# Performance work log

Measured on AMD Instinct MI355X. Metric: run time of the kernel, lower is better.

## Reference

```python
import jax, jax.numpy as jnp
import numpy as np

N = 100000
E = 3200000
D_IN = 128
D_OUT = 128
ALPHA = 0.2  # LeakyReLU negative slope
LN_EPS = 1e-5


def setup_inputs() -> dict:
    key = jax.random.key(0)
    k1, k2, k3, k4, k5 = jax.random.split(key, 5)
    x = jax.random.normal(k1, (N, D_IN), dtype=jnp.float32)
    edge = jax.random.randint(k2, (2, E), 0, N, dtype=jnp.int64)
    # Linear params (kaiming-normal-ish init)
    W = jax.random.normal(k3, (D_OUT, D_IN), dtype=jnp.float32) * np.sqrt(2.0 / D_IN)
    b = jnp.zeros((D_OUT,), dtype=jnp.float32)
    # attention vector a: (2*out,)
    a = jax.random.normal(k4, (2 * D_OUT,), dtype=jnp.float32) * np.sqrt(2.0 / (2 * D_OUT))
    ln_w = jnp.ones((D_OUT,), dtype=jnp.float32)
    ln_b = jnp.zeros((D_OUT,), dtype=jnp.float32)
    return {"x": x, "W": W, "b": b, "a": a, "ln_w": ln_w, "ln_b": ln_b, "edge": edge}


def reference(x, W, b, a, ln_w, ln_b, edge):
    n = x.shape[0]
    d_out = W.shape[0]
    h = x @ W.T + b  # [N, D_OUT]
    src, dst = edge[0], edge[1]
    # a.mm(cat(h[src], h[dst]).T) == h[src] @ a1 + h[dst] @ a2
    a1, a2 = a[:d_out], a[d_out:]
    node_s1 = h @ a1  # [N]
    node_s2 = h @ a2  # [N]
    z = node_s1[src] + node_s2[dst]  # [E]
    edge_e = jnp.exp(-jax.nn.leaky_relu(z, ALPHA))  # [E]
    # sparse spmm: h_prime[i] = sum_{e: src=i} edge_e[e] * h[dst[e]]
    msgs = edge_e[:, None] * h[dst]  # [E, D_OUT]
    h_prime = jax.ops.segment_sum(msgs, src, num_segments=n)  # [N, D_OUT]
    # LayerNorm over last dim
    mu = jnp.mean(h_prime, axis=-1, keepdims=True)
    var = jnp.mean(jnp.square(h_prime - mu), axis=-1, keepdims=True)
    h_norm = (h_prime - mu) * jax.lax.rsqrt(var + LN_EPS) * ln_w + ln_b
    return jax.nn.elu(h_norm)
```

## Files before the change

### kernel.cpp

```cpp
#include <hip/hip_runtime.h>
#include <math.h>

#define D 128
#define GAT_ALPHA 0.2f
#define LN_EPS 1e-5f
#define NBMAX 400
#define CAP 9216
#define ECHUNK 16384
#define XPITCH 136

typedef __attribute__((ext_vector_type(8))) short short8;
typedef __attribute__((ext_vector_type(4))) float floatx4;

__device__ __forceinline__ unsigned short f2bf(float f) {
    unsigned u = __float_as_uint(f);
    unsigned r = (u + 0x7fffu + ((u >> 16) & 1u)) >> 16;
    return (unsigned short)r;
}
__device__ __forceinline__ float bfl(unsigned u) { return __uint_as_float(u << 16); }
__device__ __forceinline__ float bfh(unsigned u) { return __uint_as_float(u & 0xffff0000u); }

__global__ __launch_bounds__(256) void prep_bfrag(const float* __restrict__ W,
                                                  unsigned short* __restrict__ Bfrag)
{
    for (int idx = threadIdx.x; idx < 2048; idx += 256) {
        int lane = idx & 63, ntkt = idx >> 6;
        int nt = ntkt >> 2, kt = ntkt & 3;
        int l16 = lane & 15, quad = lane >> 4;
        const float* wp = W + (size_t)(nt * 16 + l16) * D + kt * 32 + quad * 8;
        unsigned short* op = Bfrag + (size_t)idx * 8;
#pragma unroll
        for (int j = 0; j < 8; ++j) op[j] = f2bf(wp[j]);
    }
}

__global__ __launch_bounds__(256) void gemm_mfma(const float* __restrict__ x,
                                                 const unsigned short* __restrict__ Bfrag_g,
                                                 const float* __restrict__ b,
                                                 const float* __restrict__ a,
                                                 unsigned short* __restrict__ h16,
                                                 float* __restrict__ s1,
                                                 float* __restrict__ s2, int n)
{
    __shared__ unsigned short Bf[16384];
    __shared__ unsigned short xs[64 * XPITCH];
    const int tid = threadIdx.x;
    {
        const uint2* sp = (const uint2*)Bfrag_g;
        uint2* dp = (uint2*)Bf;
        for (int i = tid; i < 4096; i += 256) dp[i] = sp[i];
    }
    const int row0 = blockIdx.x * 64;

    for (int i = tid; i < 2048; i += 256) {
        int row = i >> 5, c4 = i & 31;
        float4 v = make_float4(0.f, 0.f, 0.f, 0.f);
        if (row0 + row < n) v = *(const float4*)(x + (size_t)(row0 + row) * D + c4 * 4);
        ushort4 o;
        o.x = f2bf(v.x); o.y = f2bf(v.y); o.z = f2bf(v.z); o.w = f2bf(v.w);
        *(ushort4*)&xs[row * XPITCH + c4 * 4] = o;
    }
    __syncthreads();

    const int lane = tid & 63, wave = tid >> 6;
    const int l16 = lane & 15, quad = lane >> 4;

    floatx4 acc[8];
#pragma unroll
    for (int nt = 0; nt < 8; ++nt) acc[nt] = (floatx4){0.f, 0.f, 0.f, 0.f};

#pragma unroll
    for (int kt = 0; kt < 4; ++kt) {
        short8 af = *(const short8*)&xs[(wave * 16 + l16) * XPITCH + kt * 32 + quad * 8];
#pragma unroll
        for (int nt = 0; nt < 8; ++nt) {
            short8 bf = *(const short8*)&Bf[(size_t)((nt * 4 + kt) * 64 + lane) * 8];
            acc[nt] = __builtin_amdgcn_mfma_f32_16x16x32_bf16(af, bf, acc[nt], 0, 0, 0);
        }
    }

    float bcol[8], a1c[8], a2c[8];
#pragma unroll
    for (int nt = 0; nt < 8; ++nt) {
        int c = nt * 16 + l16;
        bcol[nt] = b[c]; a1c[nt] = a[c]; a2c[nt] = a[D + c];
    }
    float hv[4][8];
#pragma unroll
    for (int r = 0; r < 4; ++r) {
        float p1 = 0.f, p2 = 0.f;
#pragma unroll
        for (int nt = 0; nt < 8; ++nt) {
            float v = acc[nt][r] + bcol[nt];
            hv[r][nt] = v;
            p1 = fmaf(v, a1c[nt], p1);
            p2 = fmaf(v, a2c[nt], p2);
        }
#pragma unroll
        for (int off = 8; off > 0; off >>= 1) {
            p1 += __shfl_xor(p1, off);
            p2 += __shfl_xor(p2, off);
        }
        int crow = row0 + wave * 16 + quad * 4 + r;
        if (crow < n && l16 == 0) { s1[crow] = p1; s2[crow] = p2; }
    }

    __syncthreads();
#pragma unroll
    for (int r = 0; r < 4; ++r)
#pragma unroll
        for (int nt = 0; nt < 8; ++nt)
            xs[(wave * 16 + quad * 4 + r) * XPITCH + nt * 16 + l16] = f2bf(hv[r][nt]);
    __syncthreads();

    for (int i = tid; i < 1024; i += 256) {
        int row = i >> 4, c = i & 15;
        if (row0 + row < n)
            *(uint4*)(h16 + (size_t)(row0 + row) * D + c * 8) =
                *(const uint4*)&xs[row * XPITCH + c * 8];
    }
}

__global__ __launch_bounds__(512) void partition_kernel(const int* __restrict__ src,
                                                        const int* __restrict__ dst,
                                                        int* __restrict__ gcnt,
                                                        int* __restrict__ pairs,
                                                        int nE, int nb)
{
    __shared__ int cnt[NBMAX], basex[NBMAX], cnt2[NBMAX];
    int tid = threadIdx.x;
    for (int i = tid; i < nb; i += 512) { cnt[i] = 0; cnt2[i] = 0; }
    __syncthreads();
    int e0 = blockIdx.x * ECHUNK;
    int e1 = e0 + ECHUNK; if (e1 > nE) e1 = nE;
    for (int e = e0 + tid; e < e1; e += 512)
        atomicAdd(&cnt[src[e] >> 8], 1);
    __syncthreads();
    for (int i = tid; i < nb; i += 512)
        basex[i] = cnt[i] ? atomicAdd(&gcnt[i], cnt[i]) : 0;
    __syncthreads();
    for (int e = e0 + tid; e < e1; e += 512) {
        int s = src[e];
        int bb = s >> 8;
        int l = basex[bb] + atomicAdd(&cnt2[bb], 1);
        if (l < CAP) pairs[(size_t)bb * CAP + l] = ((s & 255) << 24) | dst[e];
    }
}

__global__ __launch_bounds__(256) void bucket_sort(const int* __restrict__ pairs,
                                                   const int* __restrict__ gcnt,
                                                   const float* __restrict__ s1,
                                                   const float* __restrict__ s2,
                                                   int* __restrict__ beg,
                                                   int* __restrict__ end_,
                                                   int2* __restrict__ csr, int n)
{
    __shared__ int cnt[256], excl[256], cnt2[256], wsum[4];
    int bkt = blockIdx.x, tid = threadIdx.x;
    int base = bkt * CAP;
    int m = gcnt[bkt]; if (m > CAP) m = CAP;
    cnt[tid] = 0; cnt2[tid] = 0;
    __syncthreads();
    for (int e = tid; e < m; e += 256)
        atomicAdd(&cnt[((unsigned)pairs[base + e]) >> 24], 1);
    __syncthreads();

    int lane = tid & 63, wid = tid >> 6;
    int v = cnt[tid], incl = v;
#pragma unroll
    for (int off = 1; off < 64; off <<= 1) {
        int t = __shfl_up(incl, off);
        if (lane >= off) incl += t;
    }
    if (lane == 63) wsum[wid] = incl;
    __syncthreads();
    int woff = 0;
#pragma unroll
    for (int w = 0; w < 4; ++w)
        if (w < wid) woff += wsum[w];
    int ex = woff + incl - v;
    excl[tid] = ex;
    int node = bkt * 256 + tid;
    if (node < n) { beg[node] = base + ex; end_[node] = base + ex + v; }
    __syncthreads();

    for (int e = tid; e < m; e += 256) {
        int w = pairs[base + e];
        int sl = ((unsigned)w) >> 24;
        int d = w & 0xFFFFFF;
        int s = (bkt << 8) | sl;
        float z = s1[s] + s2[d];
        float lz = z > 0.f ? z : GAT_ALPHA * z;
        float ee = __expf(-lz);
        int pos = excl[sl] + atomicAdd(&cnt2[sl], 1);
        csr[base + pos] = make_int2(d, __float_as_int(ee));
    }
}

__global__ __launch_bounds__(256) void aggregate_kernel(const unsigned short* __restrict__ h16,
                                                        const int* __restrict__ beg,
                                                        const int* __restrict__ end_,
                                                        const int2* __restrict__ csr,
                                                        const float* __restrict__ ln_w,
                                                        const float* __restrict__ ln_b,
                                                        float* __restrict__ out, int n)
{
    int node = blockIdx.x * 4 + (threadIdx.x >> 6);
    if (node >= n) return;
    int lane = threadIdx.x & 63;
    int q    = lane >> 4;
    int l16  = lane & 15;

    int e0 = beg[node], e1 = end_[node];

    float acc[8];
#pragma unroll
    for (int j = 0; j < 8; ++j) acc[j] = 0.f;

    int e = e0 + q;
    for (; e + 4 < e1; e += 8) {
        int2 pa = csr[e];
        int2 pb = csr[e + 4];
        const uint4* gpa = (const uint4*)(h16 + (size_t)pa.x * D + l16 * 8);
        const uint4* gpb = (const uint4*)(h16 + (size_t)pb.x * D + l16 * 8);
        uint4 ua = *gpa;
        uint4 ub = *gpb;
        float ea = __int_as_float(pa.y);
        float eb = __int_as_float(pb.y);
        acc[0] = fmaf(ea, bfl(ua.x), acc[0]);
        acc[1] = fmaf(ea, bfh(ua.x), acc[1]);
        acc[2] = fmaf(ea, bfl(ua.y), acc[2]);
        acc[3] = fmaf(ea, bfh(ua.y), acc[3]);
        acc[4] = fmaf(ea, bfl(ua.z), acc[4]);
        acc[5] = fmaf(ea, bfh(ua.z), acc[5]);
        acc[6] = fmaf(ea, bfl(ua.w), acc[6]);
        acc[7] = fmaf(ea, bfh(ua.w), acc[7]);
        acc[0] = fmaf(eb, bfl(ub.x), acc[0]);
        acc[1] = fmaf(eb, bfh(ub.x), acc[1]);
        acc[2] = fmaf(eb, bfl(ub.y), acc[2]);
        acc[3] = fmaf(eb, bfh(ub.y), acc[3]);
        acc[4] = fmaf(eb, bfl(ub.z), acc[4]);
        acc[5] = fmaf(eb, bfh(ub.z), acc[5]);
        acc[6] = fmaf(eb, bfl(ub.w), acc[6]);
        acc[7] = fmaf(eb, bfh(ub.w), acc[7]);
    }
    for (; e < e1; e += 4) {
        int2 p = csr[e];
        float ee = __int_as_float(p.y);
        uint4 u = *(const uint4*)(h16 + (size_t)p.x * D + l16 * 8);
        acc[0] = fmaf(ee, bfl(u.x), acc[0]);
        acc[1] = fmaf(ee, bfh(u.x), acc[1]);
        acc[2] = fmaf(ee, bfl(u.y), acc[2]);
        acc[3] = fmaf(ee, bfh(u.y), acc[3]);
        acc[4] = fmaf(ee, bfl(u.z), acc[4]);
        acc[5] = fmaf(ee, bfh(u.z), acc[5]);
        acc[6] = fmaf(ee, bfl(u.w), acc[6]);
        acc[7] = fmaf(ee, bfh(u.w), acc[7]);
    }
#pragma unroll
    for (int j = 0; j < 8; ++j) acc[j] += __shfl_down(acc[j], 32);
#pragma unroll
    for (int j = 0; j < 8; ++j) acc[j] += __shfl_down(acc[j], 16);

    float sum = 0.f, sq = 0.f;
#pragma unroll
    for (int j = 0; j < 8; ++j) { sum += acc[j]; sq += acc[j] * acc[j]; }
#pragma unroll
    for (int off = 8; off > 0; off >>= 1) {
        sum += __shfl_xor(sum, off);
        sq  += __shfl_xor(sq, off);
    }

    if (q == 0) {
        float mu   = sum * (1.0f / 128.0f);
        float var  = sq * (1.0f / 128.0f) - mu * mu;
        float rstd = rsqrtf(var + LN_EPS);

        float4 w0 = *(const float4*)(ln_w + l16 * 8);
        float4 w1 = *(const float4*)(ln_w + l16 * 8 + 4);
        float4 b0 = *(const float4*)(ln_b + l16 * 8);
        float4 b1 = *(const float4*)(ln_b + l16 * 8 + 4);
        float y[8];
        y[0] = (acc[0] - mu) * rstd * w0.x + b0.x;
        y[1] = (acc[1] - mu) * rstd * w0.y + b0.y;
        y[2] = (acc[2] - mu) * rstd * w0.z + b0.z;
        y[3] = (acc[3] - mu) * rstd * w0.w + b0.w;
        y[4] = (acc[4] - mu) * rstd * w1.x + b1.x;
        y[5] = (acc[5] - mu) * rstd * w1.y + b1.y;
        y[6] = (acc[6] - mu) * rstd * w1.z + b1.z;
        y[7] = (acc[7] - mu) * rstd * w1.w + b1.w;
#pragma unroll
        for (int j = 0; j < 8; ++j) y[j] = y[j] > 0.f ? y[j] : expm1f(y[j]);
        float* op = out + (size_t)node * D + l16 * 8;
        *(float4*)op       = make_float4(y[0], y[1], y[2], y[3]);
        *(float4*)(op + 4) = make_float4(y[4], y[5], y[6], y[7]);
    }
}

extern "C" void kernel_launch(void* const* d_in, const int* in_sizes, int n_in,
                              void* d_out, int out_size, void* d_ws, size_t ws_size,
                              hipStream_t stream)
{
    const float* x    = (const float*)d_in[0];
    const float* W    = (const float*)d_in[1];
    const float* b    = (const float*)d_in[2];
    const float* a    = (const float*)d_in[3];
    const float* ln_w = (const float*)d_in[4];
    const float* ln_b = (const float*)d_in[5];
    const int*   edge = (const int*)d_in[6];

    const int n  = in_sizes[0] / D;
    const int nE = in_sizes[6] / 2;
    const int* src = edge;
    const int* dst = edge + nE;
    const int nb = (n + 255) >> 8;

    float* out = (float*)d_out;

    unsigned short* h16 = (unsigned short*)d_ws;
    float* s1   = (float*)(h16 + (size_t)n * D);
    float* s2   = s1 + n;
    unsigned short* Bfrag = (unsigned short*)(s2 + n);
    int* pairs  = (int*)(Bfrag + 16384);
    int2* csr   = (int2*)(pairs + (size_t)nb * CAP);
    int* beg    = (int*)(csr + (size_t)nb * CAP);
    int* end_   = beg + n;
    int* gcnt   = end_ + n;

    hipMemsetAsync(gcnt, 0, (size_t)nb * sizeof(int), stream);

    prep_bfrag      <<<1, 256, 0, stream>>>(W, Bfrag);
    gemm_mfma       <<<(n + 63) / 64, 256, 0, stream>>>(x, Bfrag, b, a, h16, s1, s2, n);
    partition_kernel<<<(nE + ECHUNK - 1) / ECHUNK, 512, 0, stream>>>(src, dst, gcnt, pairs, nE, nb);
    bucket_sort     <<<nb, 256, 0, stream>>>(pairs, gcnt, s1, s2, beg, end_, csr, n);
    aggregate_kernel<<<(n + 3) / 4, 256, 0, stream>>>(h16, beg, end_, csr, ln_w, ln_b, out, n);
}
```

Before: 362.7 us.

## Fuse bucket sort with aggregation using LDS-resident CSR and 128-node buckets

Merges the bucket_sort and aggregate kernels into a single kernel per 128-node bucket. Each block builds the sorted edge list in shared memory and then aggregates, normalises and writes the output for its nodes. This drops the global CSR write and read, the beg/end arrays and one launch, and caches s1 for the bucket in shared memory. The GEMM also now processes two 64-row tiles per block so each block loads the B fragments once for both. The costs are a large LDS footprint per block (about 38KB), fewer resident blocks (782 buckets), and a per-bucket capacity of 4736 edges that overflows if a bucket receives more edges than that.

```diff
diff --git a/kernel.cpp b/kernel.cpp
--- a/kernel.cpp
+++ b/kernel.cpp
@@ -4,8 +4,8 @@
 #define D 128
 #define GAT_ALPHA 0.2f
 #define LN_EPS 1e-5f
-#define NBMAX 400
-#define CAP 9216
+#define NB2MAX 800
+#define CAP2 4736
 #define ECHUNK 16384
 #define XPITCH 136
 
@@ -50,34 +50,8 @@
         uint2* dp = (uint2*)Bf;
         for (int i = tid; i < 4096; i += 256) dp[i] = sp[i];
     }
-    const int row0 = blockIdx.x * 64;
-
-    for (int i = tid; i < 2048; i += 256) {
-        int row = i >> 5, c4 = i & 31;
-        float4 v = make_float4(0.f, 0.f, 0.f, 0.f);
-        if (row0 + row < n) v = *(const float4*)(x + (size_t)(row0 + row) * D + c4 * 4);
-        ushort4 o;
-        o.x = f2bf(v.x); o.y = f2bf(v.y); o.z = f2bf(v.z); o.w = f2bf(v.w);
-        *(ushort4*)&xs[row * XPITCH + c4 * 4] = o;
-    }
-    __syncthreads();
-
     const int lane = tid & 63, wave = tid >> 6;
     const int l16 = lane & 15, quad = lane >> 4;
-
-    floatx4 acc[8];
-#pragma unroll
-    for (int nt = 0; nt < 8; ++nt) acc[nt] = (floatx4){0.f, 0.f, 0.f, 0.f};
-
-#pragma unroll
-    for (int kt = 0; kt < 4; ++kt) {
-        short8 af = *(const short8*)&xs[(wave * 16 + l16) * XPITCH + kt * 32 + quad * 8];
-#pragma unroll
-        for (int nt = 0; nt < 8; ++nt) {
-            short8 bf = *(const short8*)&Bf[(size_t)((nt * 4 + kt) * 64 + lane) * 8];
-            acc[nt] = __builtin_amdgcn_mfma_f32_16x16x32_bf16(af, bf, acc[nt], 0, 0, 0);
-        }
-    }
 
     float bcol[8], a1c[8], a2c[8];
 #pragma unroll
@@ -85,39 +59,69 @@
         int c = nt * 16 + l16;
         bcol[nt] = b[c]; a1c[nt] = a[c]; a2c[nt] = a[D + c];
     }
-    float hv[4][8];
-#pragma unroll
-    for (int r = 0; r < 4; ++r) {
-        float p1 = 0.f, p2 = 0.f;
-#pragma unroll
-        for (int nt = 0; nt < 8; ++nt) {
-            float v = acc[nt][r] + bcol[nt];
-            hv[r][nt] = v;
-            p1 = fmaf(v, a1c[nt], p1);
-            p2 = fmaf(v, a2c[nt], p2);
-        }
-#pragma unroll
-        for (int off = 8; off > 0; off >>= 1) {
-            p1 += __shfl_xor(p1, off);
-            p2 += __shfl_xor(p2, off);
-        }
-        int crow = row0 + wave * 16 + quad * 4 + r;
-        if (crow < n && l16 == 0) { s1[crow] = p1; s2[crow] = p2; }
-    }
-
-    __syncthreads();
-#pragma unroll
-    for (int r = 0; r < 4; ++r)
-#pragma unroll
-        for (int nt = 0; nt < 8; ++nt)
-            xs[(wave * 16 + quad * 4 + r) * XPITCH + nt * 16 + l16] = f2bf(hv[r][nt]);
-    __syncthreads();
-
-    for (int i = tid; i < 1024; i += 256) {
-        int row = i >> 4, c = i & 15;
-        if (row0 + row < n)
-            *(uint4*)(h16 + (size_t)(row0 + row) * D + c * 8) =
-                *(const uint4*)&xs[row * XPITCH + c * 8];
+
+    for (int t = 0; t < 2; ++t) {
+        const int row0 = blockIdx.x * 128 + t * 64;
+        __syncthreads();
+
+        for (int i = tid; i < 2048; i += 256) {
+            int row = i >> 5, c4 = i & 31;
+            float4 v = make_float4(0.f, 0.f, 0.f, 0.f);
+            if (row0 + row < n) v = *(const float4*)(x + (size_t)(row0 + row) * D + c4 * 4);
+            ushort4 o;
+            o.x = f2bf(v.x); o.y = f2bf(v.y); o.z = f2bf(v.z); o.w = f2bf(v.w);
+            *(ushort4*)&xs[row * XPITCH + c4 * 4] = o;
+        }
+        __syncthreads();
+
+        floatx4 acc[8];
+#pragma unroll
+        for (int nt = 0; nt < 8; ++nt) acc[nt] = (floatx4){0.f, 0.f, 0.f, 0.f};
+
+#pragma unroll
+        for (int kt = 0; kt < 4; ++kt) {
+            short8 af = *(const short8*)&xs[(wave * 16 + l16) * XPITCH + kt * 32 + quad * 8];
+#pragma unroll
+            for (int nt = 0; nt < 8; ++nt) {
+                short8 bf = *(const short8*)&Bf[(size_t)((nt * 4 + kt) * 64 + lane) * 8];
+                acc[nt] = __builtin_amdgcn_mfma_f32_16x16x32_bf16(af, bf, acc[nt], 0, 0, 0);
+            }
+        }
+
+        float hv[4][8];
+#pragma unroll
+        for (int r = 0; r < 4; ++r) {
+            float p1 = 0.f, p2 = 0.f;
+#pragma unroll
+            for (int nt = 0; nt < 8; ++nt) {
+                float v = acc[nt][r] + bcol[nt];
+                hv[r][nt] = v;
+                p1 = fmaf(v, a1c[nt], p1);
+                p2 = fmaf(v, a2c[nt], p2);
+            }
+#pragma unroll
+            for (int off = 8; off > 0; off >>= 1) {
+                p1 += __shfl_xor(p1, off);
+                p2 += __shfl_xor(p2, off);
+            }
+            int crow = row0 + wave * 16 + quad * 4 + r;
+            if (crow < n && l16 == 0) { s1[crow] = p1; s2[crow] = p2; }
+        }
+
+        __syncthreads();
+#pragma unroll
+        for (int r = 0; r < 4; ++r)
+#pragma unroll
+            for (int nt = 0; nt < 8; ++nt)
+                xs[(wave * 16 + quad * 4 + r) * XPITCH + nt * 16 + l16] = f2bf(hv[r][nt]);
+        __syncthreads();
+
+        for (int i = tid; i < 1024; i += 256) {
+            int row = i >> 4, c = i & 15;
+            if (row0 + row < n)
+                *(uint4*)(h16 + (size_t)(row0 + row) * D + c * 8) =
+                    *(const uint4*)&xs[row * XPITCH + c * 8];
+        }
     }
 }
 
@@ -127,173 +131,174 @@
                                                         int* __restrict__ pairs,
                                                         int nE, int nb)
 {
-    __shared__ int cnt[NBMAX], basex[NBMAX], cnt2[NBMAX];
+    __shared__ int cnt[NB2MAX], basex[NB2MAX], cnt2x[NB2MAX];
     int tid = threadIdx.x;
-    for (int i = tid; i < nb; i += 512) { cnt[i] = 0; cnt2[i] = 0; }
+    for (int i = tid; i < nb; i += 512) { cnt[i] = 0; cnt2x[i] = 0; }
     __syncthreads();
     int e0 = blockIdx.x * ECHUNK;
     int e1 = e0 + ECHUNK; if (e1 > nE) e1 = nE;
     for (int e = e0 + tid; e < e1; e += 512)
-        atomicAdd(&cnt[src[e] >> 8], 1);
+        atomicAdd(&cnt[src[e] >> 7], 1);
     __syncthreads();
     for (int i = tid; i < nb; i += 512)
         basex[i] = cnt[i] ? atomicAdd(&gcnt[i], cnt[i]) : 0;
     __syncthreads();
     for (int e = e0 + tid; e < e1; e += 512) {
         int s = src[e];
-        int bb = s >> 8;
-        int l = basex[bb] + atomicAdd(&cnt2[bb], 1);
-        if (l < CAP) pairs[(size_t)bb * CAP + l] = ((s & 255) << 24) | dst[e];
-    }
-}
-
-__global__ __launch_bounds__(256) void bucket_sort(const int* __restrict__ pairs,
-                                                   const int* __restrict__ gcnt,
-                                                   const float* __restrict__ s1,
-                                                   const float* __restrict__ s2,
-                                                   int* __restrict__ beg,
-                                                   int* __restrict__ end_,
-                                                   int2* __restrict__ csr, int n)
-{
-    __shared__ int cnt[256], excl[256], cnt2[256], wsum[4];
-    int bkt = blockIdx.x, tid = threadIdx.x;
-    int base = bkt * CAP;
-    int m = gcnt[bkt]; if (m > CAP) m = CAP;
-    cnt[tid] = 0; cnt2[tid] = 0;
-    __syncthreads();
-    for (int e = tid; e < m; e += 256)
+        int bb = s >> 7;
+        int l = basex[bb] + atomicAdd(&cnt2x[bb], 1);
+        if (l < CAP2) pairs[(size_t)bb * CAP2 + l] = ((s & 127) << 24) | dst[e];
+    }
+}
+
+__global__ __launch_bounds__(512, 8) void sort_aggregate(const int* __restrict__ pairs,
+                                                         const int* __restrict__ gcnt,
+                                                         const float* __restrict__ s1,
+                                                         const float* __restrict__ s2,
+                                                         const unsigned short* __restrict__ h16,
+                                                         const float* __restrict__ ln_w,
+                                                         const float* __restrict__ ln_b,
+                                                         float* __restrict__ out, int n)
+{
+    __shared__ int2 csr2[CAP2];
+    __shared__ int cnt[128], cnt2[128], excl[129];
+    __shared__ float sA[128];
+    __shared__ int wsum[2];
+
+    const int bkt = blockIdx.x, tid = threadIdx.x;
+    const int base = bkt * CAP2;
+    int m = gcnt[bkt]; if (m > CAP2) m = CAP2;
+
+    if (tid < 128) {
+        cnt[tid] = 0; cnt2[tid] = 0;
+        int node = bkt * 128 + tid;
+        sA[tid] = (node < n) ? s1[node] : 0.f;
+    }
+    __syncthreads();
+
+    for (int e = tid; e < m; e += 512)
         atomicAdd(&cnt[((unsigned)pairs[base + e]) >> 24], 1);
     __syncthreads();
 
-    int lane = tid & 63, wid = tid >> 6;
-    int v = cnt[tid], incl = v;
-#pragma unroll
-    for (int off = 1; off < 64; off <<= 1) {
-        int t = __shfl_up(incl, off);
-        if (lane >= off) incl += t;
-    }
-    if (lane == 63) wsum[wid] = incl;
-    __syncthreads();
-    int woff = 0;
-#pragma unroll
-    for (int w = 0; w < 4; ++w)
-        if (w < wid) woff += wsum[w];
-    int ex = woff + incl - v;
-    excl[tid] = ex;
-    int node = bkt * 256 + tid;
-    if (node < n) { beg[node] = base + ex; end_[node] = base + ex + v; }
-    __syncthreads();
-
-    for (int e = tid; e < m; e += 256) {
+    {
+        int lane = tid & 63, wid = tid >> 6;
+        int v = 0, incl = 0;
+        if (tid < 128) {
+            v = cnt[tid]; incl = v;
+#pragma unroll
+            for (int off = 1; off < 64; off <<= 1) {
+                int t = __shfl_up(incl, off);
+                if (lane >= off) incl += t;
+            }
+            if (lane == 63) wsum[wid] = incl;
+        }
+        __syncthreads();
+        if (tid < 128) excl[tid] = ((wid == 1) ? wsum[0] : 0) + incl - v;
+        if (tid == 0) excl[128] = wsum[0] + wsum[1];
+        __syncthreads();
+    }
+
+    for (int e = tid; e < m; e += 512) {
         int w = pairs[base + e];
         int sl = ((unsigned)w) >> 24;
         int d = w & 0xFFFFFF;
-        int s = (bkt << 8) | sl;
-        float z = s1[s] + s2[d];
+        float z = sA[sl] + s2[d];
         float lz = z > 0.f ? z : GAT_ALPHA * z;
         float ee = __expf(-lz);
         int pos = excl[sl] + atomicAdd(&cnt2[sl], 1);
-        csr[base + pos] = make_int2(d, __float_as_int(ee));
-    }
-}
-
-__global__ __launch_bounds__(256) void aggregate_kernel(const unsigned short* __restrict__ h16,
-                                                        const int* __restrict__ beg,
-                                                        const int* __restrict__ end_,
-                                                        const int2* __restrict__ csr,
-                                                        const float* __restrict__ ln_w,
-                                                        const float* __restrict__ ln_b,
-                                                        float* __restrict__ out, int n)
-{
-    int node = blockIdx.x * 4 + (threadIdx.x >> 6);
-    if (node >= n) return;
-    int lane = threadIdx.x & 63;
-    int q    = lane >> 4;
-    int l16  = lane & 15;
-
-    int e0 = beg[node], e1 = end_[node];
-
-    float acc[8];
-#pragma unroll
-    for (int j = 0; j < 8; ++j) acc[j] = 0.f;
-
-    int e = e0 + q;
-    for (; e + 4 < e1; e += 8) {
-        int2 pa = csr[e];
-        int2 pb = csr[e + 4];
-        const uint4* gpa = (const uint4*)(h16 + (size_t)pa.x * D + l16 * 8);
-        const uint4* gpb = (const uint4*)(h16 + (size_t)pb.x * D + l16 * 8);
-        uint4 ua = *gpa;
-        uint4 ub = *gpb;
-        float ea = __int_as_float(pa.y);
-        float eb = __int_as_float(pb.y);
-        acc[0] = fmaf(ea, bfl(ua.x), acc[0]);
-        acc[1] = fmaf(ea, bfh(ua.x), acc[1]);
-        acc[2] = fmaf(ea, bfl(ua.y), acc[2]);
-        acc[3] = fmaf(ea, bfh(ua.y), acc[3]);
-        acc[4] = fmaf(ea, bfl(ua.z), acc[4]);
-        acc[5] = fmaf(ea, bfh(ua.z), acc[5]);
-        acc[6] = fmaf(ea, bfl(ua.w), acc[6]);
-        acc[7] = fmaf(ea, bfh(ua.w), acc[7]);
-        acc[0] = fmaf(eb, bfl(ub.x), acc[0]);
-        acc[1] = fmaf(eb, bfh(ub.x), acc[1]);
-        acc[2] = fmaf(eb, bfl(ub.y), acc[2]);
-        acc[3] = fmaf(eb, bfh(ub.y), acc[3]);
-        acc[4] = fmaf(eb, bfl(ub.z), acc[4]);
-        acc[5] = fmaf(eb, bfh(ub.z), acc[5]);
-        acc[6] = fmaf(eb, bfl(ub.w), acc[6]);
-        acc[7] = fmaf(eb, bfh(ub.w), acc[7]);
-    }
-    for (; e < e1; e += 4) {
-        int2 p = csr[e];
-        float ee = __int_as_float(p.y);
-        uint4 u = *(const uint4*)(h16 + (size_t)p.x * D + l16 * 8);
-        acc[0] = fmaf(ee, bfl(u.x), acc[0]);
-        acc[1] = fmaf(ee, bfh(u.x), acc[1]);
-        acc[2] = fmaf(ee, bfl(u.y), acc[2]);
-        acc[3] = fmaf(ee, bfh(u.y), acc[3]);
-        acc[4] = fmaf(ee, bfl(u.z), acc[4]);
-        acc[5] = fmaf(ee, bfh(u.z), acc[5]);
-        acc[6] = fmaf(ee, bfl(u.w), acc[6]);
-        acc[7] = fmaf(ee, bfh(u.w), acc[7]);
-    }
-#pragma unroll
-    for (int j = 0; j < 8; ++j) acc[j] += __shfl_down(acc[j], 32);
-#pragma unroll
-    for (int j = 0; j < 8; ++j) acc[j] += __shfl_down(acc[j], 16);
-
-    float sum = 0.f, sq = 0.f;
-#pragma unroll
-    for (int j = 0; j < 8; ++j) { sum += acc[j]; sq += acc[j] * acc[j]; }
-#pragma unroll
-    for (int off = 8; off > 0; off >>= 1) {
-        sum += __shfl_xor(sum, off);
-        sq  += __shfl_xor(sq, off);
-    }
-
-    if (q == 0) {
-        float mu   = sum * (1.0f / 128.0f);
-        float var  = sq * (1.0f / 128.0f) - mu * mu;
-        float rstd = rsqrtf(var + LN_EPS);
-
-        float4 w0 = *(const float4*)(ln_w + l16 * 8);
-        float4 w1 = *(const float4*)(ln_w + l16 * 8 + 4);
-        float4 b0 = *(const float4*)(ln_b + l16 * 8);
-        float4 b1 = *(const float4*)(ln_b + l16 * 8 + 4);
-        float y[8];
-        y[0] = (acc[0] - mu) * rstd * w0.x + b0.x;
-        y[1] = (acc[1] - mu) * rstd * w0.y + b0.y;
-        y[2] = (acc[2] - mu) * rstd * w0.z + b0.z;
-        y[3] = (acc[3] - mu) * rstd * w0.w + b0.w;
-        y[4] = (acc[4] - mu) * rstd * w1.x + b1.x;
-        y[5] = (acc[5] - mu) * rstd * w1.y + b1.y;
-        y[6] = (acc[6] - mu) * rstd * w1.z + b1.z;
-        y[7] = (acc[7] - mu) * rstd * w1.w + b1.w;
-#pragma unroll
-        for (int j = 0; j < 8; ++j) y[j] = y[j] > 0.f ? y[j] : expm1f(y[j]);
-        float* op = out + (size_t)node * D + l16 * 8;
-        *(float4*)op       = make_float4(y[0], y[1], y[2], y[3]);
-        *(float4*)(op + 4) = make_float4(y[4], y[5], y[6], y[7]);
+        csr2[pos] = make_int2(d, __float_as_int(ee));
+    }
+    __syncthreads();
+
+    const int lane = tid & 63, wv = tid >> 6;
+    const int q = lane >> 4, l16 = lane & 15;
+
+    for (int i = 0; i < 16; ++i) {
+        int nl = wv * 16 + i;
+        int node = bkt * 128 + nl;
+        if (node >= n) break;
+        int e0 = excl[nl], e1 = excl[nl + 1];
+
+        float acc[8];
+#pragma unroll
+        for (int j = 0; j < 8; ++j) acc[j] = 0.f;
+
+        int e = e0 + q;
+        for (; e + 4 < e1; e += 8) {
+            int2 pa = csr2[e];
+            int2 pb = csr2[e + 4];
+            uint4 ua = *(const uint4*)(h16 + (size_t)pa.x * D + l16 * 8);
+            uint4 ub = *(const uint4*)(h16 + (size_t)pb.x * D + l16 * 8);
+            float ea = __int_as_float(pa.y);
+            float eb = __int_as_float(pb.y);
+            acc[0] = fmaf(ea, bfl(ua.x), acc[0]);
+            acc[1] = fmaf(ea, bfh(ua.x), acc[1]);
+            acc[2] = fmaf(ea, bfl(ua.y), acc[2]);
+            acc[3] = fmaf(ea, bfh(ua.y), acc[3]);
+            acc[4] = fmaf(ea, bfl(ua.z), acc[4]);
+            acc[5] = fmaf(ea, bfh(ua.z), acc[5]);
+            acc[6] = fmaf(ea, bfl(ua.w), acc[6]);
+            acc[7] = fmaf(ea, bfh(ua.w), acc[7]);
+            acc[0] = fmaf(eb, bfl(ub.x), acc[0]);
+            acc[1] = fmaf(eb, bfh(ub.x), acc[1]);
+            acc[2] = fmaf(eb, bfl(ub.y), acc[2]);
+            acc[3] = fmaf(eb, bfh(ub.y), acc[3]);
+            acc[4] = fmaf(eb, bfl(ub.z), acc[4]);
+            acc[5] = fmaf(eb, bfh(ub.z), acc[5]);
+            acc[6] = fmaf(eb, bfl(ub.w), acc[6]);
+            acc[7] = fmaf(eb, bfh(ub.w), acc[7]);
+        }
+        for (; e < e1; e += 4) {
+            int2 p = csr2[e];
+            float ee = __int_as_float(p.y);
+            uint4 u = *(const uint4*)(h16 + (size_t)p.x * D + l16 * 8);
+            acc[0] = fmaf(ee, bfl(u.x), acc[0]);
+            acc[1] = fmaf(ee, bfh(u.x), acc[1]);
+            acc[2] = fmaf(ee, bfl(u.y), acc[2]);
+            acc[3] = fmaf(ee, bfh(u.y), acc[3]);
+            acc[4] = fmaf(ee, bfl(u.z), acc[4]);
+            acc[5] = fmaf(ee, bfh(u.z), acc[5]);
+            acc[6] = fmaf(ee, bfl(u.w), acc[6]);
+            acc[7] = fmaf(ee, bfh(u.w), acc[7]);
+        }
+#pragma unroll
+        for (int j = 0; j < 8; ++j) acc[j] += __shfl_down(acc[j], 32);
+#pragma unroll
+        for (int j = 0; j < 8; ++j) acc[j] += __shfl_down(acc[j], 16);
+
+        float sum = 0.f, sq = 0.f;
+#pragma unroll
+        for (int j = 0; j < 8; ++j) { sum += acc[j]; sq += acc[j] * acc[j]; }
+#pragma unroll
+        for (int off = 8; off > 0; off >>= 1) {
+            sum += __shfl_xor(sum, off);
+            sq  += __shfl_xor(sq, off);
+        }
+
+        if (q == 0) {
+            float mu   = sum * (1.0f / 128.0f);
+            float var  = sq * (1.0f / 128.0f) - mu * mu;
+            float rstd = rsqrtf(var + LN_EPS);
+
+            float4 w0 = *(const float4*)(ln_w + l16 * 8);
+            float4 w1 = *(const float4*)(ln_w + l16 * 8 + 4);
+            float4 b0 = *(const float4*)(ln_b + l16 * 8);
+            float4 b1 = *(const float4*)(ln_b + l16 * 8 + 4);
+            float y[8];
+            y[0] = (acc[0] - mu) * rstd * w0.x + b0.x;
+            y[1] = (acc[1] - mu) * rstd * w0.y + b0.y;
+            y[2] = (acc[2] - mu) * rstd * w0.z + b0.z;
+            y[3] = (acc[3] - mu) * rstd * w0.w + b0.w;
+            y[4] = (acc[4] - mu) * rstd * w1.x + b1.x;
+            y[5] = (acc[5] - mu) * rstd * w1.y + b1.y;
+            y[6] = (acc[6] - mu) * rstd * w1.z + b1.z;
+            y[7] = (acc[7] - mu) * rstd * w1.w + b1.w;
+#pragma unroll
+            for (int j = 0; j < 8; ++j) y[j] = y[j] > 0.f ? y[j] : expm1f(y[j]);
+            float* op = out + (size_t)node * D + l16 * 8;
+            *(float4*)op       = make_float4(y[0], y[1], y[2], y[3]);
+            *(float4*)(op + 4) = make_float4(y[4], y[5], y[6], y[7]);
+        }
     }
 }
 
@@ -313,7 +318,7 @@
     const int nE = in_sizes[6] / 2;
     const int* src = edge;
     const int* dst = edge + nE;
-    const int nb = (n + 255) >> 8;
+    const int nb2 = (n + 127) >> 7;
 
     float* out = (float*)d_out;
 
@@ -322,16 +327,12 @@
     float* s2   = s1 + n;
     unsigned short* Bfrag = (unsigned short*)(s2 + n);
     int* pairs  = (int*)(Bfrag + 16384);
-    int2* csr   = (int2*)(pairs + (size_t)nb * CAP);
-    int* beg    = (int*)(csr + (size_t)nb * CAP);
-    int* end_   = beg + n;
-    int* gcnt   = end_ + n;
-
-    hipMemsetAsync(gcnt, 0, (size_t)nb * sizeof(int), stream);
+    int* gcnt   = pairs + (size_t)nb2 * CAP2;
+
+    hipMemsetAsync(gcnt, 0, (size_t)nb2 * sizeof(int), stream);
 
     prep_bfrag      <<<1, 256, 0, stream>>>(W, Bfrag);
-    gemm_mfma       <<<(n + 63) / 64, 256, 0, stream>>>(x, Bfrag, b, a, h16, s1, s2, n);
-    partition_kernel<<<(nE + ECHUNK - 1) / ECHUNK, 512, 0, stream>>>(src, dst, gcnt, pairs, nE, nb);
-    bucket_sort     <<<nb, 256, 0, stream>>>(pairs, gcnt, s1, s2, beg, end_, csr, n);
-    aggregate_kernel<<<(n + 3) / 4, 256, 0, stream>>>(h16, beg, end_, csr, ln_w, ln_b, out, n);
-}
+    gemm_mfma       <<<(n + 127) / 128, 256, 0, stream>>>(x, Bfrag, b, a, h16, s1, s2, n);
+    partition_kernel<<<(nE + ECHUNK - 1) / ECHUNK, 512, 0, stream>>>(src, dst, gcnt, pairs, nE, nb2);
+    sort_aggregate  <<<nb2, 512, 0, stream>>>(pairs, gcnt, s1, s2, h16, ln_w, ln_b, out, n);
+}
```

Result: faster. 352.6 us (-2.8%).
